# Kernel optimization log

Measured on AMD Instinct MI355X. Metric: run time of the kernel, lower is better.

## Reference

```python
import jax, jax.numpy as jnp
import numpy as np

N, E, C, EMB, NB, L = 20000, 640000, 64, 32, 8, 2
MAX_RADIUS = 2.5
NUM_NEIGHBORS = 32.0
RH = 32  # radial MLP hidden


def setup_inputs() -> dict:
    key = jax.random.key(0)
    ks = jax.random.split(key, 24)
    g = lambda k, shape, fan: (jax.random.normal(k, shape, dtype=jnp.float32) / np.sqrt(fan).astype(np.float32))
    inp = {
        'x': jax.random.normal(ks[0], (N, 6), dtype=jnp.float32),
        'batch': jnp.zeros((N,), dtype=jnp.int64),
        'node_attr': jax.random.randint(ks[1], (N,), 0, 100),
        'edge_src': jax.random.randint(ks[2], (E,), 0, N),
        'edge_dst': jax.random.randint(ks[3], (E,), 0, N),
        'emb_table': jax.random.normal(ks[4], (100, EMB), dtype=jnp.float32),
        'uplift_M': jax.random.normal(ks[5], (C, 2), dtype=jnp.float32),
        'h': jnp.ones((L,), jnp.float32) * 0.01,
        'mix': jnp.ones((L,), jnp.float32) * 0.5,
        'rad_W1': g(ks[6], (L, NB, RH), NB),
        'rad_b1': jnp.zeros((L, RH), jnp.float32),
        'rad_W2': g(ks[7], (L, RH, 2 * C), RH),
        'lin1_s': g(ks[8], (L, C, C), C),
        'lin1_v': g(ks[9], (L, C, C), C),
        'lin2_s': g(ks[10], (L, C, 2 * C), C),
        'lin2_v': g(ks[11], (L, C, C), C),
        'sc_s_w': g(ks[12], (L, C, EMB, 2 * C), C * EMB),
        'sc_v_w': g(ks[13], (L, C, EMB, C), C * EMB),
        'si_s': g(ks[14], (L, C, C), C),
        'si_v': g(ks[15], (L, C, C), C),
    }
    return inp


def _forward(x, batch, node_attr, edge_src, edge_dst, emb_table, uplift_M, h, mix,
             rad_W1, rad_b1, rad_W2, lin1_s, lin1_v, lin2_s, lin2_v,
             sc_s_w, sc_v_w, si_s, si_v):
    n = x.shape[0]
    emb = emb_table[node_attr]                       # [N, EMB] node embedding
    # semi-unitarize uplift matrix: Q = M (M^T M)^{-1/2} == U V^T
    U, _, Vt = jnp.linalg.svd(uplift_M, full_matrices=False)
    Q = U @ Vt                                       # [C, 2]
    xv = x.reshape(n, 2, 3)
    y_s = jnp.zeros((n, C), x.dtype)                 # hidden scalars start at 0
    y_v = jnp.einsum('nkx,ck->ncx', xv, Q)           # uplift vectors [N,C,3]
    y = (y_s, y_v)
    y_old = y
    nbas = jnp.arange(1, NB + 1, dtype=x.dtype)
    inv_nn = 1.0 / np.sqrt(NUM_NEIGHBORS).astype(np.float32)
    for i in range(L):
        pos = x[:, :3]
        ev = pos[edge_src] - pos[edge_dst]           # [E,3]
        elen = jnp.linalg.norm(ev, axis=1)
        safe = jnp.maximum(elen, 1e-9)
        sh = np.float32(np.sqrt(3.0)) * ev / safe[:, None]   # 1x1o SH, component norm
        # bessel radial basis, scaled by sqrt(NB)
        ef = (np.float32(np.sqrt(2.0 / MAX_RADIUS)) *
              jnp.sin(nbas[None, :] * jnp.pi * safe[:, None] / MAX_RADIUS) / safe[:, None])
        ef = ef * np.float32(np.sqrt(NB))
        # smooth cutoff (e3nn tetris style)
        u = 2.0 * (elen / MAX_RADIUS - 1.0)
        cut = jnp.where(u > 0, 0.0, jnp.where(u < -2, 1.0, 0.5 * (1.0 - jnp.cos(jnp.pi * u))))
        ea = cut[:, None] * sh                       # [E,3] edge attr
        # linear pre-mix
        s1 = y[0] @ lin1_s[i]                        # [N,C]
        v1 = jnp.einsum('ncx,cd->ndx', y[1], lin1_v[i])  # [N,C,3]
        # radial MLP -> per-edge TP weights
        w = jax.nn.silu(ef @ rad_W1[i] + rad_b1[i]) @ rad_W2[i]  # [E,2C]
        w1, w2 = w[:, :C], w[:, C:]
        # tensor-product messages: 0e x 1o -> 1o ; 1o . 1o -> 0e
        msg_v = (w1 * s1[edge_src])[:, :, None] * ea[:, None, :]        # [E,C,3]
        msg_s = w2 * jnp.einsum('ecx,ex->ec', v1[edge_src], ea)         # [E,C]
        agg_s = jax.ops.segment_sum(msg_s, edge_dst, num_segments=n) * inv_nn
        agg_v = jax.ops.segment_sum(msg_v, edge_dst, num_segments=n) * inv_nn
        # post linear + node-attr self connection
        out_s = agg_s @ lin2_s[i] + jnp.einsum('nc,ne,ceo->no', y[0], emb, sc_s_w[i])   # [N,2C]
        out_v = (jnp.einsum('ncx,cd->ndx', agg_v, lin2_v[i]) +
                 jnp.einsum('ncx,ne,ceo->nox', y[1], emb, sc_v_w[i]))                   # [N,C,3]
        # gated nonlinearity
        g_s = jax.nn.silu(out_s[:, :C])
        g_v = jax.nn.sigmoid(out_s[:, C:])[:, :, None] * out_v
        # self interaction
        y2_s = y[0] @ si_s[i]
        y2_v = jnp.einsum('ncx,cd->ndx', y[1], si_v[i])
        # leapfrog update
        hh = h[i] * h[i]
        m = mix[i]
        new_s = 2.0 * y[0] - y_old[0] + hh * (m * g_s + (m - 1.0) * y2_s)
        new_v = 2.0 * y[1] - y_old[1] + hh * (m * g_v + (m - 1.0) * y2_v)
        y_old = y
        y = (new_s, new_v)
        x = jnp.einsum('ncx,ck->nkx', new_v, Q).reshape(n, 6)   # project
    return x


def reference(x, batch, node_attr, edge_src, edge_dst, emb_table, uplift_M, h, mix,
              rad_W1, rad_b1, rad_W2, lin1_s, lin1_v, lin2_s, lin2_v,
              sc_s_w, sc_v_w, si_s, si_v):
    return _forward(x, batch, node_attr, edge_src, edge_dst, emb_table, uplift_M, h, mix,
                    rad_W1, rad_b1, rad_W2, lin1_s, lin1_v, lin2_s, lin2_v,
                    sc_s_w, sc_v_w, si_s, si_v)
```

## Files before the change

### kernel.cpp

```cpp
#include <hip/hip_runtime.h>
#include <cstdio>
#include <cstdint>

#define CCH 64
#define EMBD 32
#define NBD 8
#define RHD 32
#define NATTR 100
#define TBINS 64

static constexpr float MAXR    = 2.5f;
static constexpr float INVNN   = 0.17677669529663687f;
static constexpr float EFK     = 2.5298221281347035f;
static constexpr float SQRT3   = 1.7320508075688772f;
static constexpr float PI_F    = 3.14159265358979323846f;

__device__ __forceinline__ float sigm_(float x) { return 1.f / (1.f + __expf(-x)); }
__device__ __forceinline__ float silu_(float x) { return x / (1.f + __expf(-x)); }
__device__ __forceinline__ unsigned f2bfu(float f) {
    unsigned u = __float_as_uint(f);
    return (u + 0x7FFF + ((u >> 16) & 1)) >> 16;
}
__device__ __forceinline__ unsigned pack2(float lo, float hi) {
    return f2bfu(lo) | (f2bfu(hi) << 16);
}
__device__ __forceinline__ float ulo(unsigned u) { return __uint_as_float(u << 16); }
__device__ __forceinline__ float uhi(unsigned u) { return __uint_as_float(u & 0xFFFF0000u); }

__global__ void kQ(const float* M, float* Q) {
    int c = threadIdx.x;
    float m0 = M[2*c], m1 = M[2*c+1];
    float a = m0*m0, b = m0*m1, d = m1*m1;
    for (int o = 32; o > 0; o >>= 1) {
        a += __shfl_xor(a, o); b += __shfl_xor(b, o); d += __shfl_xor(d, o);
    }
    float det = a*d - b*b;
    float s = sqrtf(det);
    float t = sqrtf(a + d + 2.f*s);
    float inv = 1.f / (s*t);
    float i00 = (d + s)*inv, i01 = -b*inv, i11 = (a + s)*inv;
    Q[2*c]   = m0*i00 + m1*i01;
    Q[2*c+1] = m0*i01 + m1*i11;
}

__global__ void kRadTab(const float* __restrict__ rW1, const float* __restrict__ rb1,
                        const float* __restrict__ rW2, unsigned* __restrict__ tab) {
    int bin = blockIdx.x;
    int l   = blockIdx.y;
    int lane = threadIdx.x;
    float r = bin * (MAXR / TBINS);
    float safe = fmaxf(r, 1e-9f);
    float invSafe = 1.f / safe;
    float th = PI_F * r * (1.f / MAXR);
    float s0, c0;
    __sincosf(th, &s0, &c0);
    __shared__ float hidS[RHD];
    if (lane < RHD) {
        float hs = rb1[l*RHD + lane];
        float sPrev = 0.f, sCur = s0, twoC = 2.f*c0;
        #pragma unroll
        for (int b = 0; b < NBD; ++b) {
            float efb = EFK * sCur * invSafe;
            hs = fmaf(efb, rW1[(l*NBD + b)*RHD + lane], hs);
            float sN = fmaf(twoC, sCur, -sPrev);
            sPrev = sCur; sCur = sN;
        }
        hidS[lane] = silu_(hs);
    }
    __syncthreads();
    float w1 = 0.f, w2 = 0.f;
    #pragma unroll
    for (int rr = 0; rr < RHD; ++rr) {
        float h = hidS[rr];
        w1 = fmaf(h, rW2[(l*RHD + rr)*128 + lane], w1);
        w2 = fmaf(h, rW2[(l*RHD + rr)*128 + 64 + lane], w2);
    }
    float cut = s0*s0;
    float coef = SQRT3 * cut * invSafe;
    tab[((size_t)l*(TBINS+1) + bin)*64 + lane] = pack2(w1*coef, w2*coef);
}

__global__ __launch_bounds__(256) void kInitLin(const float* __restrict__ x, const float* __restrict__ Qg,
        const float* __restrict__ L1v,
        float* __restrict__ yAs, float* __restrict__ yAv, float4* __restrict__ pos4,
        uint2* __restrict__ mv, int n) {
    __shared__ unsigned wPk[32*64];
    __shared__ uint2 bc[4][64];
    int t = threadIdx.x;
    for (int i = t; i < 32*64; i += 256) {
        int cp = i >> 6, o = i & 63;
        wPk[i] = pack2(L1v[(2*cp)*64 + o], L1v[(2*cp+1)*64 + o]);
    }
    __syncthreads();
    int lane = t & 63;
    int wid = t >> 6;
    float q0 = Qg[2*lane], q1 = Qg[2*lane+1];
    for (int node = blockIdx.x*4 + wid; node < n; node += gridDim.x*4) {
        const float* xr = x + (size_t)node*6;
        float x0 = xr[0], x1 = xr[1], x2 = xr[2], x3 = xr[3], x4 = xr[4], x5 = xr[5];
        float y0 = q0*x0 + q1*x3;
        float y1 = q0*x1 + q1*x4;
        float y2 = q0*x2 + q1*x5;
        float* yv = yAv + (size_t)node*192 + lane*3;
        yv[0] = y0; yv[1] = y1; yv[2] = y2;
        yAs[(size_t)node*64 + lane] = 0.f;
        if (lane == 0) pos4[node] = (float4){x0, x1, x2, 0.f};
        bc[wid][lane] = (uint2){ pack2(y0, y1), pack2(y2, 0.f) };
        float a0A=0.f, a0B=0.f, a1A=0.f, a1B=0.f, a2A=0.f, a2B=0.f;
        #pragma unroll 8
        for (int cp = 0; cp < 32; ++cp) {
            int c = 2*cp;
            uint2 b0 = bc[wid][c];
            uint2 b1 = bc[wid][c+1];
            unsigned wp = wPk[cp*64 + lane];
            float wv0 = ulo(wp), wv1 = uhi(wp);
            a0A = fmaf(ulo(b0.x), wv0, a0A); a0B = fmaf(ulo(b1.x), wv1, a0B);
            a1A = fmaf(uhi(b0.x), wv0, a1A); a1B = fmaf(uhi(b1.x), wv1, a1B);
            a2A = fmaf(ulo(b0.y), wv0, a2A); a2B = fmaf(ulo(b1.y), wv1, a2B);
        }
        mv[(size_t)node*64 + lane] =
            (uint2){ pack2(a0A+a0B, a1A+a1B), pack2(a2A+a2B, 0.f) };
    }
}

__global__ void kHist(const int* dst, int* cnt, int e) {
    int i = blockIdx.x*blockDim.x + threadIdx.x;
    if (i < e) atomicAdd(&cnt[dst[i]], 1);
}

__global__ void kScan(const int* cnt, int* offs, int* cursor, int n) {
    __shared__ int part[1024];
    int t = threadIdx.x;
    int chunk = (n + 1023) >> 10;
    int lo = t*chunk, hi = min(lo + chunk, n);
    int s = 0;
    for (int i = lo; i < hi; ++i) s += cnt[i];
    part[t] = s;
    __syncthreads();
    for (int o = 1; o < 1024; o <<= 1) {
        int w = (t >= o) ? part[t - o] : 0;
        __syncthreads();
        part[t] += w;
        __syncthreads();
    }
    int run = part[t] - s;
    for (int i = lo; i < hi; ++i) {
        int cv = cnt[i];
        offs[i] = run; cursor[i] = run;
        run += cv;
    }
    if (t == 1023) offs[n] = part[1023];
}

__global__ void kScatter(const int* src, const int* dst, int* cursor,
                         int* srcSorted, int e) {
    int i = blockIdx.x*blockDim.x + threadIdx.x;
    if (i < e) {
        int p = atomicAdd(&cursor[dst[i]], 1);
        srcSorted[p] = src[i];
    }
}

__global__ __launch_bounds__(256) void kT3(const float* __restrict__ embT,
        const float* __restrict__ scs, const float* __restrict__ scv,
        unsigned* __restrict__ Tsp, unsigned* __restrict__ Tvp) {
    int cp = blockIdx.x, l = blockIdx.y, ag = blockIdx.z;
    int c0 = 2*cp, c1 = c0 + 1;
    __shared__ float sS0[32*128], sS1[32*128], sV0[32*64], sV1[32*64], sE[20*EMBD];
    int t = threadIdx.x;
    const float* p0 = scs + ((size_t)(l*CCH + c0)*EMBD)*128;
    const float* p1 = scs + ((size_t)(l*CCH + c1)*EMBD)*128;
    for (int i = t; i < 32*128; i += 256) { sS0[i] = p0[i]; sS1[i] = p1[i]; }
    const float* q0 = scv + ((size_t)(l*CCH + c0)*EMBD)*64;
    const float* q1 = scv + ((size_t)(l*CCH + c1)*EMBD)*64;
    for (int i = t; i < 32*64; i += 256) { sV0[i] = q0[i]; sV1[i] = q1[i]; }
    const float* eb = embT + (size_t)ag*20*EMBD;
    for (int i = t; i < 20*EMBD; i += 256) sE[i] = eb[i];
    __syncthreads();
    if (t < 128) {
        int o = t;
        for (int a = 0; a < 20; ++a) {
            float acc0 = 0.f, acc1 = 0.f;
            #pragma unroll
            for (int e = 0; e < EMBD; ++e) {
                float ev = sE[a*EMBD + e];
                acc0 = fmaf(ev, sS0[e*128 + o], acc0);
                acc1 = fmaf(ev, sS1[e*128 + o], acc1);
            }
            int aa = ag*20 + a;
            Tsp[(((size_t)l*NATTR + aa)*32 + cp)*128 + o] = pack2(acc0, acc1);
        }
    } else if (t < 192) {
        int o = t - 128;
        for (int a = 0; a < 20; ++a) {
            float acc0 = 0.f, acc1 = 0.f;
            #pragma unroll
            for (int e = 0; e < EMBD; ++e) {
                float ev = sE[a*EMBD + e];
                acc0 = fmaf(ev, sV0[e*64 + o], acc0);
                acc1 = fmaf(ev, sV1[e*64 + o], acc1);
            }
            int aa = ag*20 + a;
            Tvp[(((size_t)l*NATTR + aa)*32 + cp)*64 + o] = pack2(acc0, acc1);
        }
    }
}

__global__ __launch_bounds__(256) void kLin1(const float* __restrict__ ys, const float* __restrict__ yv,
        const float* __restrict__ L1s, const float* __restrict__ L1v,
        uint2* __restrict__ mv, int n) {
    __shared__ uint2 wPk[32*64];
    __shared__ uint2 bc[4][64];
    int t = threadIdx.x;
    for (int i = t; i < 32*64; i += 256) {
        int cp = i >> 6, o = i & 63;
        wPk[i] = (uint2){ pack2(L1s[(2*cp)*64 + o], L1s[(2*cp+1)*64 + o]),
                          pack2(L1v[(2*cp)*64 + o], L1v[(2*cp+1)*64 + o]) };
    }
    __syncthreads();
    int lane = t & 63;
    int wid = t >> 6;
    for (int node = blockIdx.x*4 + wid; node < n; node += gridDim.x*4) {
        float ys_r = ys[(size_t)node*64 + lane];
        const float* yvp = yv + (size_t)node*192 + lane*3;
        float y0 = yvp[0], y1 = yvp[1], y2 = yvp[2];
        bc[wid][lane] = (uint2){ pack2(y0, y1), pack2(y2, ys_r) };
        float asA=0.f, asB=0.f, a0A=0.f, a0B=0.f, a1A=0.f, a1B=0.f, a2A=0.f, a2B=0.f;
        #pragma unroll 8
        for (int cp = 0; cp < 32; ++cp) {
            int c = 2*cp;
            uint2 b0 = bc[wid][c];
            uint2 b1 = bc[wid][c+1];
            uint2 wp = wPk[cp*64 + lane];
            float ws0 = ulo(wp.x), ws1 = uhi(wp.x);
            float wv0 = ulo(wp.y), wv1 = uhi(wp.y);
            asA = fmaf(uhi(b0.y), ws0, asA); asB = fmaf(uhi(b1.y), ws1, asB);
            a0A = fmaf(ulo(b0.x), wv0, a0A); a0B = fmaf(ulo(b1.x), wv1, a0B);
            a1A = fmaf(uhi(b0.x), wv0, a1A); a1B = fmaf(uhi(b1.x), wv1, a1B);
            a2A = fmaf(ulo(b0.y), wv0, a2A); a2B = fmaf(ulo(b1.y), wv1, a2B);
        }
        mv[(size_t)node*64 + lane] =
            (uint2){ pack2(a0A+a0B, a1A+a1B), pack2(a2A+a2B, asA+asB) };
    }
}

template<int WITHV>
__global__ __launch_bounds__(256) void kAgg(const float4* __restrict__ pos4,
        const uint2* __restrict__ mv,
        const int* __restrict__ offs, const int* __restrict__ srcSorted,
        const unsigned* __restrict__ tabG,
        float* __restrict__ aggS, float* __restrict__ aggV, int n) {
    __shared__ unsigned tab[(TBINS+1)*64];
    __shared__ float red[4][64][4];
    int t = threadIdx.x;
    for (int i = t; i < (TBINS+1)*64; i += 256) tab[i] = tabG[i];
    __syncthreads();
    int lane = t & 63;
    int wid = t >> 6;

    for (int node = blockIdx.x; node < n; node += gridDim.x) {
        float4 pc = pos4[node];
        float px = pc.x, py = pc.y, pz = pc.z;
        int beg = offs[node], end = offs[node+1];
        float accS = 0.f, av0 = 0.f, av1 = 0.f, av2 = 0.f;
        int idx = beg + wid;
        int srcA = 0, srcB = 0;
        float4 pA = (float4){0.f,0.f,0.f,0.f};
        if (idx < end) srcA = srcSorted[idx];
        if (idx + 4 < end) srcB = srcSorted[idx + 4];
        if (idx < end) pA = pos4[srcA];
        for (; idx < end; idx += 4) {
            int srcU = srcA;
            float ex = pA.x - px, ey = pA.y - py, ez = pA.z - pz;
            srcA = srcB;
            if (idx + 8 < end) srcB = srcSorted[idx + 8];
            if (idx + 4 < end) pA = pos4[srcA];
            float el2 = ex*ex + ey*ey + ez*ez;
            if (el2 >= MAXR*MAXR) continue;
            uint2 mw = mv[(size_t)srcU*64 + lane];
            float elen = sqrtf(el2);
            float u = elen * ((float)TBINS / MAXR);
            int i0 = (int)u;
            float fr = u - (float)i0;
            unsigned t0 = tab[i0*64 + lane];
            unsigned t1 = tab[i0*64 + 64 + lane];
            float w1 = fmaf(fr, ulo(t1) - ulo(t0), ulo(t0));
            float w2 = fmaf(fr, uhi(t1) - uhi(t0), uhi(t0));
            float vv0 = ulo(mw.x), vv1 = uhi(mw.x), vv2 = ulo(mw.y);
            float dv = vv0*ex + vv1*ey + vv2*ez;
            accS = fmaf(w2, dv, accS);
            if (WITHV) {
                float tt = w1 * uhi(mw.y);
                av0 = fmaf(tt, ex, av0); av1 = fmaf(tt, ey, av1); av2 = fmaf(tt, ez, av2);
            }
        }
        red[wid][lane][0] = accS; red[wid][lane][1] = av0;
        red[wid][lane][2] = av1;  red[wid][lane][3] = av2;
        __syncthreads();
        if (wid == 0) {
            float rs = red[0][lane][0] + red[1][lane][0] + red[2][lane][0] + red[3][lane][0];
            aggS[(size_t)node*64 + lane] = rs*INVNN;
            float r0 = red[0][lane][1] + red[1][lane][1] + red[2][lane][1] + red[3][lane][1];
            float r1 = red[0][lane][2] + red[1][lane][2] + red[2][lane][2] + red[3][lane][2];
            float r2 = red[0][lane][3] + red[1][lane][3] + red[2][lane][3] + red[3][lane][3];
            float* ap = aggV + (size_t)node*192 + lane*3;
            ap[0] = r0*INVNN; ap[1] = r1*INVNN; ap[2] = r2*INVNN;
        }
        __syncthreads();
    }
}

__global__ __launch_bounds__(256) void kOutComb(const float* __restrict__ ys, const float* __restrict__ yv,
        const float* __restrict__ yolds, const float* __restrict__ yoldv,
        const float* __restrict__ aggS, const float* __restrict__ aggV, const int* __restrict__ attr,
        const float* __restrict__ L2s, const float* __restrict__ L2v,
        const unsigned* __restrict__ Tsp, const unsigned* __restrict__ Tvp,
        const float* __restrict__ siS, const float* __restrict__ siV, const float* __restrict__ Qg,
        const float* __restrict__ hArr, const float* __restrict__ mArr, int li,
        float* __restrict__ newS, float* __restrict__ newV,
        float4* __restrict__ pos4out, float* __restrict__ xout6,
        int writeY, int n) {
    __shared__ uint2 wAB[32*64];
    __shared__ uint2 wLS[32*64];
    __shared__ unsigned wSv[32*64];
    __shared__ uint4 bcast[4][64];
    int t = threadIdx.x;
    for (int i = t; i < 32*64; i += 256) {
        int cp = i >> 6, o = i & 63;
        wAB[i] = (uint2){ pack2(L2s[(2*cp)*128 + o],      L2s[(2*cp+1)*128 + o]),
                          pack2(L2s[(2*cp)*128 + 64 + o], L2s[(2*cp+1)*128 + 64 + o]) };
        wLS[i] = (uint2){ pack2(L2v[(2*cp)*64 + o], L2v[(2*cp+1)*64 + o]),
                          pack2(siS[(2*cp)*64 + o], siS[(2*cp+1)*64 + o]) };
        wSv[i] = pack2(siV[(2*cp)*64 + o], siV[(2*cp+1)*64 + o]);
    }
    __syncthreads();
    int lane = t & 63;
    int wid = t >> 6;
    float hh = hArr[li]; hh *= hh;
    float m = mArr[li];
    float q0 = Qg[2*lane], q1 = Qg[2*lane+1];
    for (int node = blockIdx.x*4 + wid; node < n; node += gridDim.x*4) {
        int a = attr[node];
        const unsigned* tS = Tsp + (size_t)a*32*128;
        const unsigned* tV = Tvp + (size_t)a*32*64;
        float as_r = aggS[(size_t)node*64 + lane];
        float ys_r = ys[(size_t)node*64 + lane];
        const float* avp = aggV + (size_t)node*192 + lane*3;
        float av0 = avp[0], av1 = avp[1], av2 = avp[2];
        const float* yvp = yv + (size_t)node*192 + lane*3;
        float by0 = yvp[0], by1 = yvp[1], by2 = yvp[2];
        bcast[wid][lane] = (uint4){ pack2(as_r, ys_r), pack2(av0, by0),
                                    pack2(av1, by1),   pack2(av2, by2) };
        float oS0A=0.f,oS0B=0.f, oS1A=0.f,oS1B=0.f;
        float ov0A=0.f,ov0B=0.f, ov1A=0.f,ov1B=0.f, ov2A=0.f,ov2B=0.f;
        float q2sA=0.f,q2sB=0.f, qv0A=0.f,qv0B=0.f, qv1A=0.f,qv1B=0.f, qv2A=0.f,qv2B=0.f;
        #pragma unroll 4
        for (int cp = 0; cp < 32; ++cp) {
            int c = 2*cp;
            uint4 b0 = bcast[wid][c];
            uint4 b1 = bcast[wid][c+1];
            float asc0 = ulo(b0.x), ysc0 = uhi(b0.x);
            float asc1 = ulo(b1.x), ysc1 = uhi(b1.x);
            float a00 = ulo(b0.y), b00 = uhi(b0.y);
            float a10 = ulo(b1.y), b10 = uhi(b1.y);
            float a01 = ulo(b0.z), b01 = uhi(b0.z);
            float a11 = ulo(b1.z), b11 = uhi(b1.z);
            float a02 = ulo(b0.w), b02 = uhi(b0.w);
            float a12 = ulo(b1.w), b12 = uhi(b1.w);
            uint2 ab = wAB[cp*64 + lane];
            uint2 ls = wLS[cp*64 + lane];
            unsigned sv = wSv[cp*64 + lane];
            unsigned ts0 = tS[cp*128 + lane];
            unsigned ts1 = tS[cp*128 + 64 + lane];
            unsigned tvw = tV[cp*64 + lane];
            float lsa0 = ulo(ab.x), lsa1 = uhi(ab.x);
            float lsb0 = ulo(ab.y), lsb1 = uhi(ab.y);
            float lv0 = ulo(ls.x), lv1 = uhi(ls.x);
            float ws0 = ulo(ls.y), ws1 = uhi(ls.y);
            float wv0 = ulo(sv), wv1 = uhi(sv);
            float tsa0 = ulo(ts0), tsa1 = uhi(ts0);
            float tsb0 = ulo(ts1), tsb1 = uhi(ts1);
            float tv0 = ulo(tvw), tv1 = uhi(tvw);
            oS0A = fmaf(asc0, lsa0, fmaf(ysc0, tsa0, oS0A));
            oS0B = fmaf(asc1, lsa1, fmaf(ysc1, tsa1, oS0B));
            oS1A = fmaf(asc0, lsb0, fmaf(ysc0, tsb0, oS1A));
            oS1B = fmaf(asc1, lsb1, fmaf(ysc1, tsb1, oS1B));
            ov0A = fmaf(a00, lv0, fmaf(b00, tv0, ov0A));
            ov0B = fmaf(a10, lv1, fmaf(b10, tv1, ov0B));
            ov1A = fmaf(a01, lv0, fmaf(b01, tv0, ov1A));
            ov1B = fmaf(a11, lv1, fmaf(b11, tv1, ov1B));
            ov2A = fmaf(a02, lv0, fmaf(b02, tv0, ov2A));
            ov2B = fmaf(a12, lv1, fmaf(b12, tv1, ov2B));
            q2sA = fmaf(ysc0, ws0, q2sA); q2sB = fmaf(ysc1, ws1, q2sB);
            qv0A = fmaf(b00, wv0, qv0A);  qv0B = fmaf(b10, wv1, qv0B);
            qv1A = fmaf(b01, wv0, qv1A);  qv1B = fmaf(b11, wv1, qv1B);
            qv2A = fmaf(b02, wv0, qv2A);  qv2B = fmaf(b12, wv1, qv2B);
        }
        float gs = silu_(oS0A + oS0B);
        float sg = sigm_(oS1A + oS1B);
        float gv0 = sg*(ov0A+ov0B), gv1 = sg*(ov1A+ov1B), gv2 = sg*(ov2A+ov2B);
        float q2s = q2sA+q2sB, qv0 = qv0A+qv0B, qv1 = qv1A+qv1B, qv2 = qv2A+qv2B;
        float yos = yolds[(size_t)node*64 + lane];
        const float* yop = yoldv + (size_t)node*192 + lane*3;
        float ns  = 2.f*ys_r - yos   + hh*(m*gs  + (m-1.f)*q2s);
        float nv0 = 2.f*by0 - yop[0] + hh*(m*gv0 + (m-1.f)*qv0);
        float nv1 = 2.f*by1 - yop[1] + hh*(m*gv1 + (m-1.f)*qv1);
        float nv2 = 2.f*by2 - yop[2] + hh*(m*gv2 + (m-1.f)*qv2);
        if (writeY) {
            newS[(size_t)node*64 + lane] = ns;
            float* np = newV + (size_t)node*192 + lane*3;
            np[0] = nv0; np[1] = nv1; np[2] = nv2;
        }
        float p00 = nv0*q0, p01 = nv1*q0, p02 = nv2*q0;
        float p10 = nv0*q1, p11 = nv1*q1, p12 = nv2*q1;
        for (int o = 32; o > 0; o >>= 1) {
            p00 += __shfl_xor(p00, o); p01 += __shfl_xor(p01, o); p02 += __shfl_xor(p02, o);
            p10 += __shfl_xor(p10, o); p11 += __shfl_xor(p11, o); p12 += __shfl_xor(p12, o);
        }
        if (lane == 0) {
            if (writeY) {
                pos4out[node] = (float4){p00, p01, p02, 0.f};
            } else {
                float* xp = xout6 + (size_t)node*6;
                xp[0] = p00; xp[1] = p01; xp[2] = p02;
                xp[3] = p10; xp[4] = p11; xp[5] = p12;
            }
        }
    }
}

extern "C" void kernel_launch(void* const* d_in, const int* in_sizes, int n_in,
                              void* d_out, int out_size, void* d_ws, size_t ws_size,
                              hipStream_t stream) {
    const float* x        = (const float*)d_in[0];
    const int*   nattr    = (const int*)  d_in[2];
    const int*   esrc     = (const int*)  d_in[3];
    const int*   edst     = (const int*)  d_in[4];
    const float* embT     = (const float*)d_in[5];
    const float* upM      = (const float*)d_in[6];
    const float* hArr     = (const float*)d_in[7];
    const float* mArr     = (const float*)d_in[8];
    const float* rW1      = (const float*)d_in[9];
    const float* rb1      = (const float*)d_in[10];
    const float* rW2      = (const float*)d_in[11];
    const float* l1s      = (const float*)d_in[12];
    const float* l1v      = (const float*)d_in[13];
    const float* l2s      = (const float*)d_in[14];
    const float* l2v      = (const float*)d_in[15];
    const float* scs      = (const float*)d_in[16];
    const float* scv      = (const float*)d_in[17];
    const float* sis      = (const float*)d_in[18];
    const float* siv      = (const float*)d_in[19];
    int n = in_sizes[0] / 6;
    int e = in_sizes[3];
    float* out = (float*)d_out;

    float* w = (float*)d_ws;
    float* Q    = w; w += 128;
    float* yAs  = w; w += (size_t)n*64;
    float* yAv  = w; w += (size_t)n*192;
    float* yBs  = w; w += (size_t)n*64;
    float* yBv  = w; w += (size_t)n*192;
    float* aggS = w; w += (size_t)n*64;
    float* aggV = w; w += (size_t)n*192;
    float4* pos4 = (float4*)w; w += (size_t)n*4;
    uint2* mv    = (uint2*)w;  w += (size_t)n*128;
    unsigned* Tsp = (unsigned*)w; w += (size_t)2*NATTR*32*128;
    unsigned* Tvp = (unsigned*)w; w += (size_t)2*NATTR*32*64;
    unsigned* radTab = (unsigned*)w; w += (size_t)2*(TBINS+1)*64;
    int* cnt       = (int*)w;
    int* offs      = cnt + n;
    int* cursor    = offs + (n + 1);
    int* srcSorted = cursor + n;
    size_t need = (size_t)((char*)(srcSorted + e) - (char*)d_ws);
    if (need > ws_size) {
        fprintf(stderr, "kernel_launch: ws too small (%zu > %zu)\n", need, ws_size);
        return;
    }

    const int AGG_GRID  = 1792;
    const int OC_GRID   = 768;
    const int LIN_GRID  = 2048;

    kQ<<<1, 64, 0, stream>>>(upM, Q);
    hipMemsetAsync(cnt, 0, (size_t)n*sizeof(int), stream);
    kHist<<<(e + 255)/256, 256, 0, stream>>>(edst, cnt, e);
    kScan<<<1, 1024, 0, stream>>>(cnt, offs, cursor, n);
    kScatter<<<(e + 255)/256, 256, 0, stream>>>(esrc, edst, cursor, srcSorted, e);
    kT3<<<dim3(32, 2, 5), 256, 0, stream>>>(embT, scs, scv, Tsp, Tvp);
    kRadTab<<<dim3(TBINS+1, 2), 64, 0, stream>>>(rW1, rb1, rW2, radTab);
    kInitLin<<<LIN_GRID, 256, 0, stream>>>(x, Q, l1v, yAs, yAv, pos4, mv, n);

    kAgg<0><<<AGG_GRID, 256, 0, stream>>>(pos4, mv, offs, srcSorted,
                                  radTab, aggS, aggV, n);
    kOutComb<<<OC_GRID, 256, 0, stream>>>(yAs, yAv, yAs, yAv, aggS, aggV, nattr,
                                  l2s, l2v, Tsp, Tvp, sis, siv, Q, hArr, mArr, 0,
                                  yBs, yBv, pos4, out, 1, n);
    kLin1<<<LIN_GRID, 256, 0, stream>>>(yBs, yBv, l1s + 4096, l1v + 4096, mv, n);
    kAgg<1><<<AGG_GRID, 256, 0, stream>>>(pos4, mv, offs, srcSorted,
                                  radTab + (size_t)(TBINS+1)*64, aggS, aggV, n);
    kOutComb<<<OC_GRID, 256, 0, stream>>>(yBs, yBv, yAs, yAv, aggS, aggV, nattr,
                                  l2s + (size_t)64*128, l2v + (size_t)64*64,
                                  Tsp + (size_t)NATTR*32*128, Tvp + (size_t)NATTR*32*64,
                                  sis + 4096, siv + 4096, Q, hArr, mArr, 1,
                                  yAs, yAv, pos4, out, 0, n);
}
```

Measured before the change: 575.0 us.

## Use one wave per node in aggregation, packed fp32 math, global siV weights

The aggregation kernel now assigns one wavefront per destination node instead of one block per node. This removes the shared-memory cross-wave reduction and both block barriers, and adds software prefetch of the next edge's source, position and message. The linear and output-combine kernels switch paired accumulators to 2-wide float vectors so the compiler can emit packed FMA instructions. The siV self-interaction weight is pre-packed once into global memory and read from there, which frees shared memory so more blocks fit per CU; grid sizes and launch bounds are raised to match. The risks are load imbalance across waves for nodes of differing degree, and extra global and L2 traffic for the siV reads.

```diff
diff --git a/kernel.cpp b/kernel.cpp
--- a/kernel.cpp
+++ b/kernel.cpp
@@ -14,6 +14,8 @@
 static constexpr float EFK     = 2.5298221281347035f;
 static constexpr float SQRT3   = 1.7320508075688772f;
 static constexpr float PI_F    = 3.14159265358979323846f;
+
+typedef float v2f __attribute__((ext_vector_type(2)));
 
 __device__ __forceinline__ float sigm_(float x) { return 1.f / (1.f + __expf(-x)); }
 __device__ __forceinline__ float silu_(float x) { return x / (1.f + __expf(-x)); }
@@ -80,6 +82,13 @@
     tab[((size_t)l*(TBINS+1) + bin)*64 + lane] = pack2(w1*coef, w2*coef);
 }
 
+__global__ void kPackW(const float* __restrict__ siv, unsigned* __restrict__ siVp) {
+    int l = blockIdx.y;
+    int i = blockIdx.x*256 + threadIdx.x;
+    int cp = i >> 6, o = i & 63;
+    siVp[l*2048 + i] = pack2(siv[l*4096 + (2*cp)*64 + o], siv[l*4096 + (2*cp+1)*64 + o]);
+}
+
 __global__ __launch_bounds__(256) void kInitLin(const float* __restrict__ x, const float* __restrict__ Qg,
         const float* __restrict__ L1v,
         float* __restrict__ yAs, float* __restrict__ yAv, float4* __restrict__ pos4,
@@ -106,20 +115,20 @@
         yAs[(size_t)node*64 + lane] = 0.f;
         if (lane == 0) pos4[node] = (float4){x0, x1, x2, 0.f};
         bc[wid][lane] = (uint2){ pack2(y0, y1), pack2(y2, 0.f) };
-        float a0A=0.f, a0B=0.f, a1A=0.f, a1B=0.f, a2A=0.f, a2B=0.f;
+        v2f a0 = (v2f){0.f,0.f}, a1 = (v2f){0.f,0.f}, a2 = (v2f){0.f,0.f};
         #pragma unroll 8
         for (int cp = 0; cp < 32; ++cp) {
             int c = 2*cp;
             uint2 b0 = bc[wid][c];
             uint2 b1 = bc[wid][c+1];
             unsigned wp = wPk[cp*64 + lane];
-            float wv0 = ulo(wp), wv1 = uhi(wp);
-            a0A = fmaf(ulo(b0.x), wv0, a0A); a0B = fmaf(ulo(b1.x), wv1, a0B);
-            a1A = fmaf(uhi(b0.x), wv0, a1A); a1B = fmaf(uhi(b1.x), wv1, a1B);
-            a2A = fmaf(ulo(b0.y), wv0, a2A); a2B = fmaf(ulo(b1.y), wv1, a2B);
+            v2f wv = (v2f){ulo(wp), uhi(wp)};
+            a0 += ((v2f){ulo(b0.x), ulo(b1.x)}) * wv;
+            a1 += ((v2f){uhi(b0.x), uhi(b1.x)}) * wv;
+            a2 += ((v2f){ulo(b0.y), ulo(b1.y)}) * wv;
         }
         mv[(size_t)node*64 + lane] =
-            (uint2){ pack2(a0A+a0B, a1A+a1B), pack2(a2A+a2B, 0.f) };
+            (uint2){ pack2(a0.x+a0.y, a1.x+a1.y), pack2(a2.x+a2.y, 0.f) };
     }
 }
 
@@ -225,88 +234,95 @@
         const float* yvp = yv + (size_t)node*192 + lane*3;
         float y0 = yvp[0], y1 = yvp[1], y2 = yvp[2];
         bc[wid][lane] = (uint2){ pack2(y0, y1), pack2(y2, ys_r) };
-        float asA=0.f, asB=0.f, a0A=0.f, a0B=0.f, a1A=0.f, a1B=0.f, a2A=0.f, a2B=0.f;
+        v2f asv = (v2f){0.f,0.f}, a0 = (v2f){0.f,0.f}, a1 = (v2f){0.f,0.f}, a2 = (v2f){0.f,0.f};
         #pragma unroll 8
         for (int cp = 0; cp < 32; ++cp) {
             int c = 2*cp;
             uint2 b0 = bc[wid][c];
             uint2 b1 = bc[wid][c+1];
             uint2 wp = wPk[cp*64 + lane];
-            float ws0 = ulo(wp.x), ws1 = uhi(wp.x);
-            float wv0 = ulo(wp.y), wv1 = uhi(wp.y);
-            asA = fmaf(uhi(b0.y), ws0, asA); asB = fmaf(uhi(b1.y), ws1, asB);
-            a0A = fmaf(ulo(b0.x), wv0, a0A); a0B = fmaf(ulo(b1.x), wv1, a0B);
-            a1A = fmaf(uhi(b0.x), wv0, a1A); a1B = fmaf(uhi(b1.x), wv1, a1B);
-            a2A = fmaf(ulo(b0.y), wv0, a2A); a2B = fmaf(ulo(b1.y), wv1, a2B);
+            v2f ws = (v2f){ulo(wp.x), uhi(wp.x)};
+            v2f wv = (v2f){ulo(wp.y), uhi(wp.y)};
+            asv += ((v2f){uhi(b0.y), uhi(b1.y)}) * ws;
+            a0  += ((v2f){ulo(b0.x), ulo(b1.x)}) * wv;
+            a1  += ((v2f){uhi(b0.x), uhi(b1.x)}) * wv;
+            a2  += ((v2f){ulo(b0.y), ulo(b1.y)}) * wv;
         }
         mv[(size_t)node*64 + lane] =
-            (uint2){ pack2(a0A+a0B, a1A+a1B), pack2(a2A+a2B, asA+asB) };
+            (uint2){ pack2(a0.x+a0.y, a1.x+a1.y), pack2(a2.x+a2.y, asv.x+asv.y) };
     }
 }
 
 template<int WITHV>
-__global__ __launch_bounds__(256) void kAgg(const float4* __restrict__ pos4,
+__global__ __launch_bounds__(256, 8) void kAgg(const float4* __restrict__ pos4,
         const uint2* __restrict__ mv,
         const int* __restrict__ offs, const int* __restrict__ srcSorted,
         const unsigned* __restrict__ tabG,
         float* __restrict__ aggS, float* __restrict__ aggV, int n) {
     __shared__ unsigned tab[(TBINS+1)*64];
-    __shared__ float red[4][64][4];
     int t = threadIdx.x;
     for (int i = t; i < (TBINS+1)*64; i += 256) tab[i] = tabG[i];
     __syncthreads();
     int lane = t & 63;
     int wid = t >> 6;
 
-    for (int node = blockIdx.x; node < n; node += gridDim.x) {
+    for (int node = blockIdx.x*4 + wid; node < n; node += gridDim.x*4) {
         float4 pc = pos4[node];
         float px = pc.x, py = pc.y, pz = pc.z;
         int beg = offs[node], end = offs[node+1];
         float accS = 0.f, av0 = 0.f, av1 = 0.f, av2 = 0.f;
-        int idx = beg + wid;
-        int srcA = 0, srcB = 0;
-        float4 pA = (float4){0.f,0.f,0.f,0.f};
-        if (idx < end) srcA = srcSorted[idx];
-        if (idx + 4 < end) srcB = srcSorted[idx + 4];
-        if (idx < end) pA = pos4[srcA];
-        for (; idx < end; idx += 4) {
-            int srcU = srcA;
-            float ex = pA.x - px, ey = pA.y - py, ez = pA.z - pz;
-            srcA = srcB;
-            if (idx + 8 < end) srcB = srcSorted[idx + 8];
-            if (idx + 4 < end) pA = pos4[srcA];
-            float el2 = ex*ex + ey*ey + ez*ez;
-            if (el2 >= MAXR*MAXR) continue;
-            uint2 mw = mv[(size_t)srcU*64 + lane];
-            float elen = sqrtf(el2);
-            float u = elen * ((float)TBINS / MAXR);
-            int i0 = (int)u;
-            float fr = u - (float)i0;
-            unsigned t0 = tab[i0*64 + lane];
-            unsigned t1 = tab[i0*64 + 64 + lane];
-            float w1 = fmaf(fr, ulo(t1) - ulo(t0), ulo(t0));
-            float w2 = fmaf(fr, uhi(t1) - uhi(t0), uhi(t0));
-            float vv0 = ulo(mw.x), vv1 = uhi(mw.x), vv2 = ulo(mw.y);
-            float dv = vv0*ex + vv1*ey + vv2*ez;
-            accS = fmaf(w2, dv, accS);
-            if (WITHV) {
-                float tt = w1 * uhi(mw.y);
-                av0 = fmaf(tt, ex, av0); av1 = fmaf(tt, ey, av1); av2 = fmaf(tt, ez, av2);
+        int sN = 0, sNN = 0;
+        float4 pN = (float4){0.f,0.f,0.f,0.f};
+        float exC=0.f, eyC=0.f, ezC=0.f, el2C=0.f;
+        bool actC = false;
+        uint2 mwC = (uint2){0u,0u};
+        if (beg < end) {
+            sN = srcSorted[beg];
+            if (beg+1 < end) sNN = srcSorted[beg+1];
+            pN = pos4[sN];
+            exC = pN.x-px; eyC = pN.y-py; ezC = pN.z-pz;
+            el2C = exC*exC + eyC*eyC + ezC*ezC;
+            actC = el2C < MAXR*MAXR;
+            if (actC) mwC = mv[(size_t)sN*64 + lane];
+            sN = sNN;
+            if (beg+2 < end) sNN = srcSorted[beg+2];
+            if (beg+1 < end) pN = pos4[sN];
+        }
+        for (int i = beg; i < end; ++i) {
+            float exN=0.f, eyN=0.f, ezN=0.f, el2N=0.f;
+            bool actN = false;
+            uint2 mwN = (uint2){0u,0u};
+            if (i+1 < end) {
+                exN = pN.x-px; eyN = pN.y-py; ezN = pN.z-pz;
+                el2N = exN*exN + eyN*eyN + ezN*ezN;
+                actN = el2N < MAXR*MAXR;
+                if (actN) mwN = mv[(size_t)sN*64 + lane];
+                sN = sNN;
+                if (i+3 < end) sNN = srcSorted[i+3];
+                if (i+2 < end) pN = pos4[sN];
             }
-        }
-        red[wid][lane][0] = accS; red[wid][lane][1] = av0;
-        red[wid][lane][2] = av1;  red[wid][lane][3] = av2;
-        __syncthreads();
-        if (wid == 0) {
-            float rs = red[0][lane][0] + red[1][lane][0] + red[2][lane][0] + red[3][lane][0];
-            aggS[(size_t)node*64 + lane] = rs*INVNN;
-            float r0 = red[0][lane][1] + red[1][lane][1] + red[2][lane][1] + red[3][lane][1];
-            float r1 = red[0][lane][2] + red[1][lane][2] + red[2][lane][2] + red[3][lane][2];
-            float r2 = red[0][lane][3] + red[1][lane][3] + red[2][lane][3] + red[3][lane][3];
-            float* ap = aggV + (size_t)node*192 + lane*3;
-            ap[0] = r0*INVNN; ap[1] = r1*INVNN; ap[2] = r2*INVNN;
-        }
-        __syncthreads();
+            if (actC) {
+                float elen = sqrtf(el2C);
+                float u = elen * ((float)TBINS / MAXR);
+                int i0 = (int)u;
+                float fr = u - (float)i0;
+                unsigned t0 = tab[i0*64 + lane];
+                unsigned t1 = tab[i0*64 + 64 + lane];
+                float w1 = fmaf(fr, ulo(t1) - ulo(t0), ulo(t0));
+                float w2 = fmaf(fr, uhi(t1) - uhi(t0), uhi(t0));
+                float vv0 = ulo(mwC.x), vv1 = uhi(mwC.x), vv2 = ulo(mwC.y);
+                float dv = vv0*exC + vv1*eyC + vv2*ezC;
+                accS = fmaf(w2, dv, accS);
+                if (WITHV) {
+                    float tt = w1 * uhi(mwC.y);
+                    av0 = fmaf(tt, exC, av0); av1 = fmaf(tt, eyC, av1); av2 = fmaf(tt, ezC, av2);
+                }
+            }
+            exC=exN; eyC=eyN; ezC=ezN; el2C=el2N; actC=actN; mwC=mwN;
+        }
+        aggS[(size_t)node*64 + lane] = accS*INVNN;
+        float* ap = aggV + (size_t)node*192 + lane*3;
+        ap[0] = av0*INVNN; ap[1] = av1*INVNN; ap[2] = av2*INVNN;
     }
 }
 
@@ -315,14 +331,13 @@
         const float* __restrict__ aggS, const float* __restrict__ aggV, const int* __restrict__ attr,
         const float* __restrict__ L2s, const float* __restrict__ L2v,
         const unsigned* __restrict__ Tsp, const unsigned* __restrict__ Tvp,
-        const float* __restrict__ siS, const float* __restrict__ siV, const float* __restrict__ Qg,
+        const float* __restrict__ siS, const unsigned* __restrict__ siVp, const float* __restrict__ Qg,
         const float* __restrict__ hArr, const float* __restrict__ mArr, int li,
         float* __restrict__ newS, float* __restrict__ newV,
         float4* __restrict__ pos4out, float* __restrict__ xout6,
         int writeY, int n) {
     __shared__ uint2 wAB[32*64];
     __shared__ uint2 wLS[32*64];
-    __shared__ unsigned wSv[32*64];
     __shared__ uint4 bcast[4][64];
     int t = threadIdx.x;
     for (int i = t; i < 32*64; i += 256) {
@@ -331,7 +346,6 @@
                           pack2(L2s[(2*cp)*128 + 64 + o], L2s[(2*cp+1)*128 + 64 + o]) };
         wLS[i] = (uint2){ pack2(L2v[(2*cp)*64 + o], L2v[(2*cp+1)*64 + o]),
                           pack2(siS[(2*cp)*64 + o], siS[(2*cp+1)*64 + o]) };
-        wSv[i] = pack2(siV[(2*cp)*64 + o], siV[(2*cp+1)*64 + o]);
     }
     __syncthreads();
     int lane = t & 63;
@@ -351,61 +365,57 @@
         float by0 = yvp[0], by1 = yvp[1], by2 = yvp[2];
         bcast[wid][lane] = (uint4){ pack2(as_r, ys_r), pack2(av0, by0),
                                     pack2(av1, by1),   pack2(av2, by2) };
-        float oS0A=0.f,oS0B=0.f, oS1A=0.f,oS1B=0.f;
-        float ov0A=0.f,ov0B=0.f, ov1A=0.f,ov1B=0.f, ov2A=0.f,ov2B=0.f;
-        float q2sA=0.f,q2sB=0.f, qv0A=0.f,qv0B=0.f, qv1A=0.f,qv1B=0.f, qv2A=0.f,qv2B=0.f;
+        v2f oS0 = (v2f){0.f,0.f}, oS1 = (v2f){0.f,0.f};
+        v2f ov0 = (v2f){0.f,0.f}, ov1 = (v2f){0.f,0.f}, ov2 = (v2f){0.f,0.f};
+        v2f q2s = (v2f){0.f,0.f};
+        v2f qv0 = (v2f){0.f,0.f}, qv1 = (v2f){0.f,0.f}, qv2 = (v2f){0.f,0.f};
         #pragma unroll 4
         for (int cp = 0; cp < 32; ++cp) {
             int c = 2*cp;
             uint4 b0 = bcast[wid][c];
             uint4 b1 = bcast[wid][c+1];
-            float asc0 = ulo(b0.x), ysc0 = uhi(b0.x);
-            float asc1 = ulo(b1.x), ysc1 = uhi(b1.x);
-            float a00 = ulo(b0.y), b00 = uhi(b0.y);
-            float a10 = ulo(b1.y), b10 = uhi(b1.y);
-            float a01 = ulo(b0.z), b01 = uhi(b0.z);
-            float a11 = ulo(b1.z), b11 = uhi(b1.z);
-            float a02 = ulo(b0.w), b02 = uhi(b0.w);
-            float a12 = ulo(b1.w), b12 = uhi(b1.w);
+            v2f asc  = (v2f){ulo(b0.x), ulo(b1.x)};
+            v2f ysc  = (v2f){uhi(b0.x), uhi(b1.x)};
+            v2f av0p = (v2f){ulo(b0.y), ulo(b1.y)};
+            v2f by0p = (v2f){uhi(b0.y), uhi(b1.y)};
+            v2f av1p = (v2f){ulo(b0.z), ulo(b1.z)};
+            v2f by1p = (v2f){uhi(b0.z), uhi(b1.z)};
+            v2f av2p = (v2f){ulo(b0.w), ulo(b1.w)};
+            v2f by2p = (v2f){uhi(b0.w), uhi(b1.w)};
             uint2 ab = wAB[cp*64 + lane];
             uint2 ls = wLS[cp*64 + lane];
-            unsigned sv = wSv[cp*64 + lane];
+            unsigned sv = siVp[cp*64 + lane];
             unsigned ts0 = tS[cp*128 + lane];
             unsigned ts1 = tS[cp*128 + 64 + lane];
             unsigned tvw = tV[cp*64 + lane];
-            float lsa0 = ulo(ab.x), lsa1 = uhi(ab.x);
-            float lsb0 = ulo(ab.y), lsb1 = uhi(ab.y);
-            float lv0 = ulo(ls.x), lv1 = uhi(ls.x);
-            float ws0 = ulo(ls.y), ws1 = uhi(ls.y);
-            float wv0 = ulo(sv), wv1 = uhi(sv);
-            float tsa0 = ulo(ts0), tsa1 = uhi(ts0);
-            float tsb0 = ulo(ts1), tsb1 = uhi(ts1);
-            float tv0 = ulo(tvw), tv1 = uhi(tvw);
-            oS0A = fmaf(asc0, lsa0, fmaf(ysc0, tsa0, oS0A));
-            oS0B = fmaf(asc1, lsa1, fmaf(ysc1, tsa1, oS0B));
-            oS1A = fmaf(asc0, lsb0, fmaf(ysc0, tsb0, oS1A));
-            oS1B = fmaf(asc1, lsb1, fmaf(ysc1, tsb1, oS1B));
-            ov0A = fmaf(a00, lv0, fmaf(b00, tv0, ov0A));
-            ov0B = fmaf(a10, lv1, fmaf(b10, tv1, ov0B));
-            ov1A = fmaf(a01, lv0, fmaf(b01, tv0, ov1A));
-            ov1B = fmaf(a11, lv1, fmaf(b11, tv1, ov1B));
-            ov2A = fmaf(a02, lv0, fmaf(b02, tv0, ov2A));
-            ov2B = fmaf(a12, lv1, fmaf(b12, tv1, ov2B));
-            q2sA = fmaf(ysc0, ws0, q2sA); q2sB = fmaf(ysc1, ws1, q2sB);
-            qv0A = fmaf(b00, wv0, qv0A);  qv0B = fmaf(b10, wv1, qv0B);
-            qv1A = fmaf(b01, wv0, qv1A);  qv1B = fmaf(b11, wv1, qv1B);
-            qv2A = fmaf(b02, wv0, qv2A);  qv2B = fmaf(b12, wv1, qv2B);
-        }
-        float gs = silu_(oS0A + oS0B);
-        float sg = sigm_(oS1A + oS1B);
-        float gv0 = sg*(ov0A+ov0B), gv1 = sg*(ov1A+ov1B), gv2 = sg*(ov2A+ov2B);
-        float q2s = q2sA+q2sB, qv0 = qv0A+qv0B, qv1 = qv1A+qv1B, qv2 = qv2A+qv2B;
+            v2f lsa = (v2f){ulo(ab.x), uhi(ab.x)};
+            v2f lsb = (v2f){ulo(ab.y), uhi(ab.y)};
+            v2f lv  = (v2f){ulo(ls.x), uhi(ls.x)};
+            v2f ws  = (v2f){ulo(ls.y), uhi(ls.y)};
+            v2f wv  = (v2f){ulo(sv),   uhi(sv)};
+            v2f tsa = (v2f){ulo(ts0), uhi(ts0)};
+            v2f tsb = (v2f){ulo(ts1), uhi(ts1)};
+            v2f tv  = (v2f){ulo(tvw), uhi(tvw)};
+            oS0 += asc*lsa + ysc*tsa;
+            oS1 += asc*lsb + ysc*tsb;
+            ov0 += av0p*lv + by0p*tv;
+            ov1 += av1p*lv + by1p*tv;
+            ov2 += av2p*lv + by2p*tv;
+            q2s += ysc*ws;
+            qv0 += by0p*wv;
+            qv1 += by1p*wv;
+            qv2 += by2p*wv;
+        }
+        float gs = silu_(oS0.x + oS0.y);
+        float sg = sigm_(oS1.x + oS1.y);
+        float gv0 = sg*(ov0.x+ov0.y), gv1 = sg*(ov1.x+ov1.y), gv2 = sg*(ov2.x+ov2.y);
+        float q2sS = q2s.x+q2s.y, qv0S = qv0.x+qv0.y, qv1S = qv1.x+qv1.y, qv2S = qv2.x+qv2.y;
         float yos = yolds[(size_t)node*64 + lane];
         const float* yop = yoldv + (size_t)node*192 + lane*3;
-        float ns  = 2.f*ys_r - yos   + hh*(m*gs  + (m-1.f)*q2s);
-        float nv0 = 2.f*by0 - yop[0] + hh*(m*gv0 + (m-1.f)*qv0);
-        float nv1 = 2.f*by1 - yop[1] + hh*(m*gv1 + (m-1.f)*qv1);
-        float nv2 = 2.f*by2 - yop[2] + hh*(m*gv2 + (m-1.f)*qv2);
+        float ns  = 2.f*ys_r - yos   + hh*(m*gs  + (m-1.f)*q2sS);
+        float nv0 = 2.f*by0 - yop[0] + hh*(m*gv0 + (m-1.f)*qv0S);
+        float nv1 = 2.f*by1 - yop[1] + hh*(m*gv1 + (m-1.f)*qv1S);
+        float nv2 = 2.f*by2 - yop[2] + hh*(m*gv2 + (m-1.f)*qv2S);
         if (writeY) {
             newS[(size_t)node*64 + lane] = ns;
             float* np = newV + (size_t)node*192 + lane*3;
@@ -468,6 +478,7 @@
     unsigned* Tsp = (unsigned*)w; w += (size_t)2*NATTR*32*128;
     unsigned* Tvp = (unsigned*)w; w += (size_t)2*NATTR*32*64;
     unsigned* radTab = (unsigned*)w; w += (size_t)2*(TBINS+1)*64;
+    unsigned* siVp = (unsigned*)w; w += (size_t)2*2048;
     int* cnt       = (int*)w;
     int* offs      = cnt + n;
     int* cursor    = offs + (n + 1);
@@ -478,8 +489,8 @@
         return;
     }
 
-    const int AGG_GRID  = 1792;
-    const int OC_GRID   = 768;
+    const int AGG_GRID  = 2048;
+    const int OC_GRID   = 1024;
     const int LIN_GRID  = 2048;
 
     kQ<<<1, 64, 0, stream>>>(upM, Q);
@@ -489,12 +500,13 @@
     kScatter<<<(e + 255)/256, 256, 0, stream>>>(esrc, edst, cursor, srcSorted, e);
     kT3<<<dim3(32, 2, 5), 256, 0, stream>>>(embT, scs, scv, Tsp, Tvp);
     kRadTab<<<dim3(TBINS+1, 2), 64, 0, stream>>>(rW1, rb1, rW2, radTab);
+    kPackW<<<dim3(8, 2), 256, 0, stream>>>(siv, siVp);
     kInitLin<<<LIN_GRID, 256, 0, stream>>>(x, Q, l1v, yAs, yAv, pos4, mv, n);
 
     kAgg<0><<<AGG_GRID, 256, 0, stream>>>(pos4, mv, offs, srcSorted,
                                   radTab, aggS, aggV, n);
     kOutComb<<<OC_GRID, 256, 0, stream>>>(yAs, yAv, yAs, yAv, aggS, aggV, nattr,
-                                  l2s, l2v, Tsp, Tvp, sis, siv, Q, hArr, mArr, 0,
+                                  l2s, l2v, Tsp, Tvp, sis, siVp, Q, hArr, mArr, 0,
                                   yBs, yBv, pos4, out, 1, n);
     kLin1<<<LIN_GRID, 256, 0, stream>>>(yBs, yBv, l1s + 4096, l1v + 4096, mv, n);
     kAgg<1><<<AGG_GRID, 256, 0, stream>>>(pos4, mv, offs, srcSorted,
@@ -502,6 +514,6 @@
     kOutComb<<<OC_GRID, 256, 0, stream>>>(yBs, yBv, yAs, yAv, aggS, aggV, nattr,
                                   l2s + (size_t)64*128, l2v + (size_t)64*64,
                                   Tsp + (size_t)NATTR*32*128, Tvp + (size_t)NATTR*32*64,
-                                  sis + 4096, siv + 4096, Q, hArr, mArr, 1,
+                                  sis + 4096, siVp + 2048, Q, hArr, mArr, 1,
                                   yAs, yAv, pos4, out, 0, n);
 }
```

Result: slower. 603.8 us (+5.0%).
